# Optimization experiments

Hardware: AMD Instinct MI355X
Metric: run time of the kernel (lower is better)

Reference implementation:

```python
import jax, jax.numpy as jnp
import numpy as np
import math

B = 128      # bandwidth
BATCH = 2048 # flat batch (samples x channels)


def _dlt_weights(Bv):
    # Driscoll-Healy quadrature weights, length 2B
    k = np.arange(2 * Bv)
    p = np.arange(Bv)
    C = 2.0 / Bv * np.sin(np.pi * (2 * k + 1) / (4.0 * Bv))
    S = np.sin(np.outer(2 * k + 1, 2 * p + 1) * np.pi / (4.0 * Bv))  # [2B,B]
    return C * (S @ (1.0 / (2 * p + 1)))


def _idct_matrix(N):
    k = np.arange(N)[:, None]
    n = np.arange(N)[None, :]
    DI = np.cos(np.pi * n * (k + 0.5) / N)
    DI[:, 0] *= np.sqrt(1.0 / N)
    DI[:, 1:] *= np.sqrt(2.0 / N)
    return DI


def _idst_matrix(N):
    k = np.arange(N)[:, None]
    n = np.arange(N)[None, :]
    DI = np.sin(np.pi * (n + 1) * (k + 0.5) / N)
    DI[:, N - 1] = (-1.0) ** np.arange(N)
    DI[:, :N - 1] *= np.sqrt(2.0 / N)
    DI[:, N - 1] *= np.sqrt(1.0 / N)
    return DI


def _little_half(Bv):
    # Wigner little-d at beta=pi/2 via 3-term recurrence (vectorized over m,n)
    Bm1 = Bv - 1
    s2 = np.sqrt(2.0)
    d = np.zeros((Bv, 2 * Bv - 1, 2 * Bv - 1))
    d[0, Bm1, Bm1] = 1.0
    d[1, Bm1 - 1, Bm1 - 1] = 0.5
    d[1, Bm1 - 1, Bm1] = 1.0 / s2
    d[1, Bm1 - 1, Bm1 + 1] = 0.5
    d[1, Bm1, Bm1 - 1] = -1.0 / s2
    d[1, Bm1, Bm1 + 1] = 1.0 / s2
    d[1, Bm1 + 1, Bm1 - 1] = 0.5
    d[1, Bm1 + 1, Bm1] = -1.0 / s2
    d[1, Bm1 + 1, Bm1 + 1] = 0.5
    for l in range(2, Bv):
        m = np.arange(l).astype(np.float64)
        M, Nn = np.meshgrid(m, m, indexing='ij')
        denom = (l - 1.0) * np.sqrt((l - M) * (l + M) * (l - Nn) * (l + Nn))
        c1 = (1.0 - 2.0 * l) * M * Nn / denom
        c2 = -l * np.sqrt(((l - 1.0) ** 2 - M ** 2) * ((l - 1.0) ** 2 - Nn ** 2)) / denom
        d[l, Bm1:Bm1 + l, Bm1:Bm1 + l] = (c1 * d[l - 1, Bm1:Bm1 + l, Bm1:Bm1 + l]
                                          + c2 * d[l - 2, Bm1:Bm1 + l, Bm1:Bm1 + l])
        mm = np.arange(l + 1)
        lnV = np.array([0.5 * (math.lgamma(2 * l + 1) - math.lgamma(l + mi + 1)
                               - math.lgamma(l - mi + 1)) - l * math.log(2.0) for mi in mm])
        v = np.exp(lnV)
        d[l, Bm1 + mm, Bm1 + l] = v
        d[l, Bm1 + l, Bm1 + mm] = ((-1.0) ** (l - mm)) * v
        # symmetry fill (write order a1, a2, a3 reproduces torch loop semantics)
        sub = d[l, Bm1:Bm1 + l + 1, Bm1:Bm1 + l + 1].copy()
        M2, N2 = np.meshgrid(np.arange(l + 1), np.arange(l + 1), indexing='ij')
        a1 = ((-1.0) ** (M2 - N2)) * sub
        a2 = ((-1.0) ** (l - N2)) * sub
        a3 = ((-1.0) ** (l + M2)) * sub
        a1[0, 0] = sub[0, 0]
        a2[0, 0] = sub[0, 0]
        a3[0, 0] = sub[0, 0]
        d[l, Bm1 - l:Bm1 + 1, Bm1 - l:Bm1 + 1] = a1[::-1, ::-1]
        d[l, Bm1 - l:Bm1 + 1, Bm1:Bm1 + l + 1] = a2[::-1, :]
        d[l, Bm1:Bm1 + l + 1, Bm1 - l:Bm1 + 1] = a3[:, ::-1]
    return d


def _wigner_coeffs(Bv, d):
    Bm1 = Bv - 1
    N = 2 * Bv
    D = np.zeros((Bv, Bv, N))
    for m in range(Bv):
        for l in range(m, Bv):
            if m % 2 == 0:
                n = np.arange(l + 1)
                c = np.sqrt((2 * l + 1) / 2.0) * np.where(n == 0, np.sqrt(N), np.sqrt(2.0 * N))
                if m % 4 == 2:
                    c = -c
                coeff = c * d[l, n + Bm1, Bm1 - m] * d[l, n + Bm1, Bm1]
                coeff = np.where(np.abs(coeff) > 1e-15, coeff, 0.0)
                D[m, l, :l + 1] = coeff
            else:
                n = np.arange(l)  # n == l gives 0
                if l > 0:
                    c = np.sqrt((2 * l + 1) / 2.0) * np.sqrt(2.0 * N)
                    if m % 4 == 1:
                        c = -c
                    coeff = c * d[l, n + 1 + Bm1, Bm1 - m] * d[l, n + 1 + Bm1, Bm1]
                    coeff = np.where(np.abs(coeff) > 1e-15, coeff, 0.0)
                    D[m, l, :l] = coeff
    return D


def _buffers(Bv):
    N = 2 * Bv
    Wd = np.diag(_dlt_weights(Bv))
    XFc = Wd @ _idct_matrix(N)   # weighted DCT matrix (applied as x @ XFc)
    XFs = Wd @ _idst_matrix(N)   # weighted DST matrix
    D = _wigner_coeffs(Bv, _little_half(Bv))
    cm = ((-1.0) ** (Bv - 1)) * np.sqrt(1.0 / (2.0 * np.pi))  # Cm[B-1] scalar
    return XFc, XFs, D, cm


def setup_inputs() -> dict:
    key = jax.random.key(0)
    psiHat = jax.random.normal(key, (BATCH, B, 2 * B), dtype=jnp.float32)
    XFc, XFs, D, cm = _buffers(B)
    return {
        'psiHat': psiHat,
        'cm': jnp.float32(cm),
        'XFc': jnp.asarray(XFc, dtype=jnp.float32),
        'XFs': jnp.asarray(XFs, dtype=jnp.float32),
        'D': jnp.asarray(D, dtype=jnp.float32),
    }


def reference(psiHat, cm, XFc, XFs, D):
    # psiHat: [batch, B, 2B]; XFc/XFs: [2B, 2B]; D: [B, B, 2B]
    psi = psiHat * cm  # Cm[B-1:] broadcasts as a scalar
    # F.linear with weight = XF.T  ==  x @ XF on the last axis
    psi = psi.at[:, 0::2, :].set(jnp.einsum('bmi,ij->bmj', psi[:, 0::2, :], XFc))
    psi = psi.at[:, 1::2, :].set(jnp.einsum('bmi,ij->bmj', psi[:, 1::2, :], XFs))
    # per-order-m block matmul against Wigner coefficient blocks
    return jnp.einsum('bmi,moi->bmo', psi, D)
```

## Files before the change

### kernel.cpp

```cpp
#include <hip/hip_runtime.h>


typedef __attribute__((ext_vector_type(8))) short short8;
typedef __attribute__((ext_vector_type(4))) float f32x4;

#define NBATCH 2048
#define NM 128
#define NI 256
#define NO 128
#define BPACK_M 32768

#define NSLAB 16
#define SLABROWS 32
#define LDSBUF 32768

#define GLB(p) ((const __attribute__((address_space(1))) void*)(p))
#define LDS(p) ((__attribute__((address_space(3))) void*)(p))

__device__ __forceinline__ unsigned short f2bf(float f) {
  unsigned int u = __builtin_bit_cast(unsigned int, f);
  u += 0x7FFFu + ((u >> 16) & 1u);
  return (unsigned short)(u >> 16);
}

__device__ __forceinline__ short8 cvt8(float4 a, float4 b, float s) {
  short8 v;
  v[0] = (short)f2bf(s * a.x); v[1] = (short)f2bf(s * a.y);
  v[2] = (short)f2bf(s * a.z); v[3] = (short)f2bf(s * a.w);
  v[4] = (short)f2bf(s * b.x); v[5] = (short)f2bf(s * b.y);
  v[6] = (short)f2bf(s * b.z); v[7] = (short)f2bf(s * b.w);
  return v;
}

__global__ __launch_bounds__(256) void e_kernel(
    const float* __restrict__ XFc, const float* __restrict__ XFs,
    const float* __restrict__ D, const float* __restrict__ cmp,
    unsigned short* __restrict__ Bpack)
{
  const int m = blockIdx.x >> 1;
  const int ihalf = blockIdx.x & 1;
  const int tid = threadIdx.x;
  const int lane = tid & 63;
  const int w = tid >> 6;
  const int lr = lane & 15;
  const int lg = lane >> 4;
  const float cm = cmp[0];
  const float* __restrict__ Xp = (m & 1) ? XFs : XFc;
  const float* __restrict__ Dm = D + (size_t)m * (NO * NI);
  const int i0 = ihalf * 128 + w * 32;

  f32x4 acc[2][8];
#pragma unroll
  for (int a = 0; a < 2; a++)
#pragma unroll
    for (int b = 0; b < 8; b++) acc[a][b] = (f32x4)0.f;

  for (int kk = 0; kk < NI; kk += 32) {
    const int kb = kk + lg * 8;
    short8 af[2];
#pragma unroll
    for (int rf = 0; rf < 2; rf++) {
      const float* ap = Xp + (size_t)(i0 + rf * 16 + lr) * NI + kb;
      float4 x0 = *(const float4*)ap;
      float4 x1 = *(const float4*)(ap + 4);
      af[rf] = cvt8(x0, x1, cm);
    }
    short8 bf[8];
#pragma unroll
    for (int cf = 0; cf < 8; cf++) {
      const float* bp = Dm + (size_t)(cf * 16 + lr) * NI + kb;
      float4 x0 = *(const float4*)bp;
      float4 x1 = *(const float4*)(bp + 4);
      bf[cf] = cvt8(x0, x1, 1.0f);
    }
#pragma unroll
    for (int rf = 0; rf < 2; rf++)
#pragma unroll
      for (int cf = 0; cf < 8; cf++)
        acc[rf][cf] = __builtin_amdgcn_mfma_f32_16x16x32_bf16(
            af[rf], bf[cf], acc[rf][cf], 0, 0, 0);
  }

  unsigned short* Bm = Bpack + (size_t)m * BPACK_M;
#pragma unroll
  for (int rf = 0; rf < 2; rf++) {
    const int t = (i0 + rf * 16) >> 5;
    const int L = ((2 * rf + (lg >> 1)) & 3) * 16 + lr;
#pragma unroll
    for (int cf = 0; cf < 8; cf++) {
      ushort4 pk;
      pk.x = f2bf(acc[rf][cf][0]);
      pk.y = f2bf(acc[rf][cf][1]);
      pk.z = f2bf(acc[rf][cf][2]);
      pk.w = f2bf(acc[rf][cf][3]);
      *(ushort4*)(Bm + (size_t)(t * 8 + cf) * 512 + L * 8 + (lg & 1) * 4) = pk;
    }
  }
}

#define SB __builtin_amdgcn_sched_barrier(0)

__global__ __launch_bounds__(256, 2) void fdlt_main(
    const float* __restrict__ psiHat,
    const unsigned short* __restrict__ Bpack,
    float* __restrict__ out)
{
  __shared__ float As_f[2 * SLABROWS * 256];
  const int m = blockIdx.x;
  const int tid = threadIdx.x;
  const int lane = tid & 63;
  const int w = tid >> 6;
  const int bbase = blockIdx.y * (NSLAB * SLABROWS);
  const int lr = lane & 15;
  const int lg = lane >> 4;
  const int cfbase = (w & 1) * 4;
  char* As = (char*)As_f;

  const unsigned short* __restrict__ Bm = Bpack + (size_t)m * BPACK_M;

  short8 ball[8][4];
#pragma unroll
  for (int t = 0; t < 8; t++)
#pragma unroll
    for (int j = 0; j < 4; j++)
      ball[t][j] =
          *(const short8*)(Bm + (size_t)(t * 8 + cfbase + j) * 512 + lane * 8);

  auto STAGE = [&](int buf, int s) {
#pragma unroll
    for (int j = 0; j < 8; j++) {
      const int r = j * 4 + w;
      const int fofs = ((((lane >> 1) ^ (r & 7)) << 3) + ((lane & 1) << 2));
      const float* src =
          psiHat + ((size_t)(bbase + s * SLABROWS + r) * NM + m) * NI + fofs;
      __builtin_amdgcn_global_load_lds(GLB(src), LDS(As + buf * LDSBUF + r * 1024),
                                       16, 0, 0);
    }
  };

  const int arow = (w >> 1) * 16 + lr;
  const int rsw = lr & 7;
  f32x4 acc[4];

  STAGE(0, 0);
  STAGE(1, 1);
  asm volatile("s_waitcnt vmcnt(8)" ::: "memory");
  SB;
  __builtin_amdgcn_s_barrier();
  SB;

  for (int s = 0; s < NSLAB; s++) {
    const char* Arow = As + (s & 1) * LDSBUF + arow * 1024;
#pragma unroll
    for (int j = 0; j < 4; j++) acc[j] = (f32x4)0.f;
#pragma unroll
    for (int t = 0; t < 8; t++) {
      const int p = ((t * 4 + lg) ^ rsw) << 5;
      float4 x0 = *(const float4*)(Arow + p);
      float4 x1 = *(const float4*)(Arow + p + 16);
      short8 af = cvt8(x0, x1, 1.0f);
#pragma unroll
      for (int j = 0; j < 4; j++)
        acc[j] = __builtin_amdgcn_mfma_f32_16x16x32_bf16(
            af, ball[t][j], acc[j], 0, 0, 0);
    }

#pragma unroll
    for (int j = 0; j < 4; j++) {
      const int o = (cfbase + j) * 16 + lr;
#pragma unroll
      for (int r = 0; r < 4; r++) {
        const int b = bbase + s * SLABROWS + (w >> 1) * 16 + lg * 4 + r;
        out[((size_t)b * NM + m) * NO + o] = acc[j][r];
      }
    }

    if (s + 1 < NSLAB) {
      __builtin_amdgcn_s_barrier();
      if (s + 2 < NSLAB) {
        STAGE((s + 2) & 1, s + 2);
        asm volatile("s_waitcnt vmcnt(24)" ::: "memory");
      } else {
        asm volatile("s_waitcnt vmcnt(16)" ::: "memory");
      }
      SB;
      __builtin_amdgcn_s_barrier();
      SB;
    }
  }
}

extern "C" void kernel_launch(void* const* d_in, const int* in_sizes, int n_in,
                              void* d_out, int out_size, void* d_ws, size_t ws_size,
                              hipStream_t stream) {
  const float* psiHat = (const float*)d_in[0];
  const float* cm     = (const float*)d_in[1];
  const float* XFc    = (const float*)d_in[2];
  const float* XFs    = (const float*)d_in[3];
  const float* D      = (const float*)d_in[4];
  float* out = (float*)d_out;
  unsigned short* Bpack = (unsigned short*)d_ws;

  e_kernel<<<256, 256, 0, stream>>>(XFc, XFs, D, cm, Bpack);
  fdlt_main<<<dim3(NM, NBATCH / (NSLAB * SLABROWS)), 256, 0, stream>>>(
      psiHat, Bpack, out);
}
```

Baseline: 105.2 us.

## Use 16-row slabs with 4-deep LDS ring and single barrier per slab

Halves the slab height to 16 rows, doubling the number of slabs, and switches from a double buffer to a 4-buffer LDS ring with three slabs prefetched ahead. Each wave now covers all 16 rows and 2 output column fragments instead of 4, so it keeps fewer B-fragment registers. The pre-stage barrier is dropped, and the vmcnt accounting and XOR swizzle are reworked for the new row width. The goal is deeper prefetch of the streamed psiHat loads and fewer barrier stalls, at the cost of doing less MFMA work per LDS load and issuing more store iterations.

New measurement: 105.6 us. Within noise of the previous version (+0.4%).

```diff
diff --git a/kernel.cpp b/kernel.cpp
--- a/kernel.cpp
+++ b/kernel.cpp
@@ -10,9 +10,9 @@
 #define NO 128
 #define BPACK_M 32768
 
-#define NSLAB 16
-#define SLABROWS 32
-#define LDSBUF 32768
+#define NSLAB 32
+#define SLABROWS 16
+#define LDSBUF 16384
 
 #define GLB(p) ((const __attribute__((address_space(1))) void*)(p))
 #define LDS(p) ((__attribute__((address_space(3))) void*)(p))
@@ -105,7 +105,7 @@
     const unsigned short* __restrict__ Bpack,
     float* __restrict__ out)
 {
-  __shared__ float As_f[2 * SLABROWS * 256];
+  __shared__ float As_f[4 * SLABROWS * 256];
   const int m = blockIdx.x;
   const int tid = threadIdx.x;
   const int lane = tid & 63;
@@ -113,73 +113,77 @@
   const int bbase = blockIdx.y * (NSLAB * SLABROWS);
   const int lr = lane & 15;
   const int lg = lane >> 4;
-  const int cfbase = (w & 1) * 4;
+  const int cfbase = w * 2;
   char* As = (char*)As_f;
 
   const unsigned short* __restrict__ Bm = Bpack + (size_t)m * BPACK_M;
 
-  short8 ball[8][4];
+  short8 ball[8][2];
 #pragma unroll
   for (int t = 0; t < 8; t++)
 #pragma unroll
-    for (int j = 0; j < 4; j++)
-      ball[t][j] =
-          *(const short8*)(Bm + (size_t)(t * 8 + cfbase + j) * 512 + lane * 8);
+    for (int j = 0; j < 2; j++)
+      ball[t][j] = *(const short8*)(
+          Bm + (size_t)(t * 8 + cfbase + j) * 512 + lane * 8);
 
   auto STAGE = [&](int buf, int s) {
 #pragma unroll
-    for (int j = 0; j < 8; j++) {
+    for (int j = 0; j < 4; j++) {
       const int r = j * 4 + w;
-      const int fofs = ((((lane >> 1) ^ (r & 7)) << 3) + ((lane & 1) << 2));
+      const int fofs = ((lane ^ (r & 15)) << 2);
       const float* src =
           psiHat + ((size_t)(bbase + s * SLABROWS + r) * NM + m) * NI + fofs;
-      __builtin_amdgcn_global_load_lds(GLB(src), LDS(As + buf * LDSBUF + r * 1024),
+      __builtin_amdgcn_global_load_lds(GLB(src),
+                                       LDS(As + buf * LDSBUF + r * 1024),
                                        16, 0, 0);
     }
   };
 
-  const int arow = (w >> 1) * 16 + lr;
-  const int rsw = lr & 7;
-  f32x4 acc[4];
+  f32x4 acc[2];
 
   STAGE(0, 0);
   STAGE(1, 1);
+  STAGE(2, 2);
   asm volatile("s_waitcnt vmcnt(8)" ::: "memory");
   SB;
   __builtin_amdgcn_s_barrier();
   SB;
 
   for (int s = 0; s < NSLAB; s++) {
-    const char* Arow = As + (s & 1) * LDSBUF + arow * 1024;
-#pragma unroll
-    for (int j = 0; j < 4; j++) acc[j] = (f32x4)0.f;
+    const char* Arow = As + (s & 3) * LDSBUF + lr * 1024;
+#pragma unroll
+    for (int j = 0; j < 2; j++) acc[j] = (f32x4)0.f;
 #pragma unroll
     for (int t = 0; t < 8; t++) {
-      const int p = ((t * 4 + lg) ^ rsw) << 5;
-      float4 x0 = *(const float4*)(Arow + p);
-      float4 x1 = *(const float4*)(Arow + p + 16);
+      const int p0 = ((((t * 4 + lg) << 1) ^ lr) << 4);
+      float4 x0 = *(const float4*)(Arow + p0);
+      float4 x1 = *(const float4*)(Arow + (p0 ^ 16));
       short8 af = cvt8(x0, x1, 1.0f);
 #pragma unroll
-      for (int j = 0; j < 4; j++)
+      for (int j = 0; j < 2; j++)
         acc[j] = __builtin_amdgcn_mfma_f32_16x16x32_bf16(
             af, ball[t][j], acc[j], 0, 0, 0);
     }
 
 #pragma unroll
-    for (int j = 0; j < 4; j++) {
+    for (int j = 0; j < 2; j++) {
       const int o = (cfbase + j) * 16 + lr;
 #pragma unroll
       for (int r = 0; r < 4; r++) {
-        const int b = bbase + s * SLABROWS + (w >> 1) * 16 + lg * 4 + r;
+        const int b = bbase + s * SLABROWS + lg * 4 + r;
         out[((size_t)b * NM + m) * NO + o] = acc[j][r];
       }
     }
 
     if (s + 1 < NSLAB) {
-      __builtin_amdgcn_s_barrier();
-      if (s + 2 < NSLAB) {
-        STAGE((s + 2) & 1, s + 2);
-        asm volatile("s_waitcnt vmcnt(24)" ::: "memory");
+      if (s + 3 < NSLAB) {
+        STAGE((s + 3) & 3, s + 3);
+        if (s == 0)
+          asm volatile("s_waitcnt vmcnt(16)" ::: "memory");
+        else
+          asm volatile("s_waitcnt vmcnt(24)" ::: "memory");
+      } else if (s + 2 < NSLAB) {
+        asm volatile("s_waitcnt vmcnt(20)" ::: "memory");
       } else {
         asm volatile("s_waitcnt vmcnt(16)" ::: "memory");
       }
```
